# Performance work log

Measured on AMD Instinct MI355X. Metric: run time of the kernel, lower is better.

Reference implementation:

```python
import jax, jax.numpy as jnp
import numpy as np

EPS = 1e-5

def _rmsnorm(x, w):
    return x * jax.lax.rsqrt(jnp.mean(x * x, axis=-1, keepdims=True) + EPS) * w


def setup_inputs() -> dict:
    key = jax.random.key(0)
    ks = jax.random.split(key, 12)
    b, l, d = 2, 4096, 1024
    expand, d_state, d_conv, headdim = 2, 128, 4, 64
    d_inner = d * expand            # 2048
    nheads = d_inner // headdim     # 32
    conv_dim = d_inner + 2 * d_state            # 2304 (x, B, C; ngroups=1)
    d_in_proj = 2 * d_inner + 2 * d_state + nheads  # z, xBC, dt
    s = 0.02
    return {
        "x": jax.random.normal(ks[0], (b, l, d), jnp.float32),
        "norm_w": jnp.ones((d,), jnp.float32),
        "in_proj_W": jax.random.normal(ks[1], (d, d_in_proj), jnp.float32) * s,
        "conv_W": jax.random.normal(ks[2], (d_conv, conv_dim), jnp.float32) * s,
        "conv_b": jnp.zeros((conv_dim,), jnp.float32),
        "dt_bias": jax.random.normal(ks[3], (nheads,), jnp.float32) * 0.5,
        "A_log": jnp.log(jnp.arange(1, nheads + 1, dtype=jnp.float32)),
        "D": jnp.ones((nheads,), jnp.float32),
        "gnorm_w": jnp.ones((d_inner,), jnp.float32),
        "zero_W": jax.random.normal(ks[4], (d, d_inner), jnp.float32) * s,
        "one_W": jax.random.normal(ks[5], (d, d_inner), jnp.float32) * s,
        "fusion_W": jax.random.normal(ks[6], (3 * d_inner, d), jnp.float32) * s,
    }


def _mamba2(xn, in_proj_W, conv_W, conv_b, dt_bias, A_log, D, gnorm_w):
    b, l, _ = xn.shape
    nheads = dt_bias.shape[0]
    conv_dim = conv_W.shape[1]
    d_state = (conv_W.shape[1] - gnorm_w.shape[0]) // 2
    d_inner = gnorm_w.shape[0]
    headdim = d_inner // nheads

    zxbcdt = xn @ in_proj_W                         # (b,l, 2*d_inner+2*n+h)
    z = zxbcdt[..., :d_inner]
    xBC = zxbcdt[..., d_inner:d_inner + conv_dim]
    dt = zxbcdt[..., -nheads:]

    # causal depthwise conv over seq, kernel size d_conv
    d_conv = conv_W.shape[0]
    pad = jnp.pad(xBC, ((0, 0), (d_conv - 1, 0), (0, 0)))
    conv = conv_b
    for k in range(d_conv):
        conv = conv + pad[:, k:k + l, :] * conv_W[k]
    xBC = jax.nn.silu(conv)

    xs = xBC[..., :d_inner].reshape(b, l, nheads, headdim)   # (b,l,h,p)
    Bm = xBC[..., d_inner:d_inner + d_state]                 # (b,l,n)
    Cm = xBC[..., d_inner + d_state:]                        # (b,l,n)

    dt = jax.nn.softplus(dt + dt_bias)                       # (b,l,h)
    A = -jnp.exp(A_log)                                      # (h,)
    dA = jnp.exp(dt * A)                                     # (b,l,h)

    def step(state, inp):
        dA_t, dt_t, B_t, C_t, x_t = inp   # (b,h),(b,h),(b,n),(b,n),(b,h,p)
        state = state * dA_t[:, :, None, None] + \
            (dt_t[:, :, None] * x_t)[..., None] * B_t[:, None, None, :]
        y_t = jnp.einsum('bhpn,bn->bhp', state, C_t)
        return state, y_t

    state0 = jnp.zeros((b, nheads, headdim, d_state), xn.dtype)
    inps = (dA.transpose(1, 0, 2), dt.transpose(1, 0, 2),
            Bm.transpose(1, 0, 2), Cm.transpose(1, 0, 2),
            xs.transpose(1, 0, 2, 3))
    _, ys = jax.lax.scan(step, state0, inps)                 # (l,b,h,p)
    y = ys.transpose(1, 0, 2, 3) + D[None, None, :, None] * xs
    y = y.reshape(b, l, d_inner)
    return _rmsnorm(y * jax.nn.silu(z), gnorm_w)             # (b,l,d_inner)


def reference(x, norm_w, in_proj_W, conv_W, conv_b, dt_bias, A_log, D,
              gnorm_w, zero_W, one_W, fusion_W):
    residual = x
    xn = _rmsnorm(x, norm_w)
    mamba_out = _mamba2(xn, in_proj_W, conv_W, conv_b, dt_bias, A_log, D, gnorm_w)
    y_zero = xn @ zero_W
    y_one = jnp.cumsum(xn @ one_W, axis=1)
    fused = jnp.concatenate([mamba_out, y_zero, y_one], axis=-1)
    return residual + fused @ fusion_W
```

## Files before the change

### kernel.cpp

```cpp
#include <hip/hip_runtime.h>
#include <hip/hip_bf16.h>
#include <stdint.h>

#define BATCH   2
#define SEQL    4096
#define DMODEL  1024
#define DIN     2048
#define NH      32
#define HDIM    64
#define DSTATE  128
#define CONVD   2304
#define DPROJ   4384
#define NTOT    8192
#define NBIG    6528
#define NREAL   6432
#define CHT     128
#define NCH     32
#define SP      136

typedef __attribute__((ext_vector_type(8))) short short8;
typedef __attribute__((ext_vector_type(4))) float f32x4;

__device__ __forceinline__ unsigned short f2bf(float f) {
    unsigned int u = __builtin_bit_cast(unsigned int, f);
    return (unsigned short)((u + 0x7FFFu + ((u >> 16) & 1u)) >> 16);
}
__device__ __forceinline__ float bf2f(unsigned short u) {
    unsigned int v = ((unsigned int)u) << 16;
    return __builtin_bit_cast(float, v);
}

__device__ __forceinline__ void gload16(const void* g, void* l) {
    __builtin_amdgcn_global_load_lds(
        (const __attribute__((address_space(1))) unsigned int*)g,
        (__attribute__((address_space(3))) unsigned int*)l,
        16, 0, 0);
}

__global__ void transpose_cast_kernel(const float* __restrict__ in,
                                      unsigned short* __restrict__ out,
                                      int R, int C) {
    __shared__ float tile[32][33];
    int c0 = blockIdx.x * 32, r0 = blockIdx.y * 32;
    int tx = threadIdx.x, ty = threadIdx.y;
    #pragma unroll
    for (int i = ty; i < 32; i += 8)
        tile[i][tx] = in[(size_t)(r0 + i) * C + c0 + tx];
    __syncthreads();
    #pragma unroll
    for (int i = ty; i < 32; i += 8)
        out[(size_t)(c0 + i) * R + r0 + tx] = f2bf(tile[tx][i]);
}

__global__ void cast_bf16_kernel(const float* __restrict__ in,
                                 unsigned short* __restrict__ out, int n4) {
    int i = (blockIdx.x * 256 + threadIdx.x) * 4;
    if (i < n4) {
        float4 v = *(const float4*)(in + i);
        ushort4 o;
        o.x = f2bf(v.x); o.y = f2bf(v.y); o.z = f2bf(v.z); o.w = f2bf(v.w);
        *(ushort4*)(out + i) = o;
    }
}

__global__ void zero_pad_kernel(unsigned short* __restrict__ p, int n) {
    int i = blockIdx.x * 256 + threadIdx.x;
    if (i < n) p[i] = 0;
}

__global__ __launch_bounds__(256) void rmsnorm_cast_kernel(
    const float* __restrict__ x, const float* __restrict__ w,
    unsigned short* __restrict__ xn) {
    int tok = blockIdx.x, tid = threadIdx.x;
    float4 v = ((const float4*)(x + (size_t)tok * DMODEL))[tid];
    float ss = v.x*v.x + v.y*v.y + v.z*v.z + v.w*v.w;
    #pragma unroll
    for (int off = 32; off > 0; off >>= 1) ss += __shfl_xor(ss, off, 64);
    __shared__ float sred[4];
    if ((tid & 63) == 0) sred[tid >> 6] = ss;
    __syncthreads();
    float tot = sred[0] + sred[1] + sred[2] + sred[3];
    float r = rsqrtf(tot * (1.0f / DMODEL) + 1e-5f);
    float4 wv = ((const float4*)w)[tid];
    ushort4 o;
    o.x = f2bf(v.x * r * wv.x); o.y = f2bf(v.y * r * wv.y);
    o.z = f2bf(v.z * r * wv.z); o.w = f2bf(v.w * r * wv.w);
    ((ushort4*)(xn + (size_t)tok * DMODEL))[tid] = o;
}

template<int MODE>
__global__ __launch_bounds__(256) void gemm_bt_kernel(
    const unsigned short* __restrict__ A, int lda,
    const unsigned short* __restrict__ B, int ldb,
    void* __restrict__ Cout, int ldc, int K,
    const float* __restrict__ addX, const unsigned short* __restrict__ Zbuf) {
    __shared__ __align__(16) unsigned short sA[128 * 64];
    __shared__ __align__(16) unsigned short sB[128 * 64];
    int tid = threadIdx.x;
    int bid = blockIdx.y * gridDim.x + blockIdx.x;
    int W = gridDim.x * 8;
    int band = bid / W, rem = bid % W;
    int bn = rem >> 3, bm = band * 8 + (rem & 7);
    int wave = tid >> 6, lane = tid & 63;
    int wm = wave >> 1, wn = wave & 1;
    f32x4 acc[4][4] = {};
    const unsigned short* Ab = A + (size_t)(bm * 128) * lda;
    const unsigned short* Bb = B + (size_t)(bn * 128) * ldb;
    int sRow = tid >> 3;
    int srcoff = (((tid & 7) - (tid >> 3)) & 7) * 8;
    int quad = lane >> 4, l15 = lane & 15;
    for (int k0 = 0; k0 < K; k0 += 64) {
        __syncthreads();
        #pragma unroll
        for (int it = 0; it < 4; ++it) {
            int row = sRow + it * 32;
            gload16(&Ab[(size_t)row * lda + k0 + srcoff], &sA[it * 2048 + tid * 8]);
            gload16(&Bb[(size_t)row * ldb + k0 + srcoff], &sB[it * 2048 + tid * 8]);
        }
        __syncthreads();
        #pragma unroll
        for (int kk = 0; kk < 64; kk += 32) {
            short8 a[4], b[4];
            #pragma unroll
            for (int i = 0; i < 4; ++i) {
                int mr = wm * 64 + i * 16 + l15;
                a[i] = *(const short8*)&sA[mr * 64 + (((kk >> 3) + quad + mr) & 7) * 8];
                int nr = wn * 64 + i * 16 + l15;
                b[i] = *(const short8*)&sB[nr * 64 + (((kk >> 3) + quad + nr) & 7) * 8];
            }
            #pragma unroll
            for (int i = 0; i < 4; ++i)
                #pragma unroll
                for (int j = 0; j < 4; ++j)
                    acc[i][j] = __builtin_amdgcn_mfma_f32_16x16x32_bf16(
                        a[i], b[j], acc[i][j], 0, 0, 0);
        }
    }
    int rbase = bm * 128 + wm * 64 + quad * 4;
    int cbase = bn * 128 + wn * 64 + l15;
    #pragma unroll
    for (int i = 0; i < 4; ++i) {
        #pragma unroll
        for (int r = 0; r < 4; ++r) {
            int gr = rbase + i * 16 + r;
            if constexpr (MODE == 1) {
                unsigned short* crow = (unsigned short*)Cout + (size_t)gr * ldc + cbase;
                #pragma unroll
                for (int j = 0; j < 4; ++j) crow[j * 16] = f2bf(acc[i][j][r]);
            } else {
                float* crow = (float*)Cout + (size_t)gr * ldc + cbase;
                const float* xr = addX + (size_t)gr * DMODEL + cbase;
                const unsigned short* zrow = Zbuf + (size_t)gr * NBIG;
                const float* qrow = (const float*)zrow;
                #pragma unroll
                for (int j = 0; j < 4; ++j)
                    crow[j * 16] = acc[i][j][r] + xr[j * 16]
                                 + bf2f(zrow[4384 + cbase + j * 16])
                                 + qrow[cbase + j * 16];
            }
        }
    }
}

__global__ __launch_bounds__(256) void gemm64_kernel(
    const unsigned short* __restrict__ A, int lda,
    const unsigned short* __restrict__ B, int ldb,
    unsigned short* __restrict__ Cout, int ldc, int K) {
    __shared__ __align__(16) unsigned short sA[64 * 64];
    __shared__ __align__(16) unsigned short sB[64 * 64];
    int tid = threadIdx.x;
    int bn = blockIdx.x, bm = blockIdx.y;
    int wave = tid >> 6, lane = tid & 63;
    int wm = wave >> 1, wn = wave & 1;
    f32x4 acc[2][2] = {};
    const unsigned short* Ab = A + (size_t)(bm * 64) * lda;
    const unsigned short* Bb = B + (size_t)(bn * 64) * ldb;
    int sRow = tid >> 3;
    int srcoff = (((tid & 7) - (tid >> 3)) & 7) * 8;
    int quad = lane >> 4, l15 = lane & 15;
    for (int k0 = 0; k0 < K; k0 += 64) {
        __syncthreads();
        #pragma unroll
        for (int it = 0; it < 2; ++it) {
            int row = sRow + it * 32;
            gload16(&Ab[(size_t)row * lda + k0 + srcoff], &sA[it * 2048 + tid * 8]);
            gload16(&Bb[(size_t)row * ldb + k0 + srcoff], &sB[it * 2048 + tid * 8]);
        }
        __syncthreads();
        #pragma unroll
        for (int kk = 0; kk < 64; kk += 32) {
            short8 a[2], b[2];
            #pragma unroll
            for (int i = 0; i < 2; ++i) {
                int mr = wm * 32 + i * 16 + l15;
                a[i] = *(const short8*)&sA[mr * 64 + (((kk >> 3) + quad + mr) & 7) * 8];
                int nr = wn * 32 + i * 16 + l15;
                b[i] = *(const short8*)&sB[nr * 64 + (((kk >> 3) + quad + nr) & 7) * 8];
            }
            #pragma unroll
            for (int i = 0; i < 2; ++i)
                #pragma unroll
                for (int j = 0; j < 2; ++j)
                    acc[i][j] = __builtin_amdgcn_mfma_f32_16x16x32_bf16(
                        a[i], b[j], acc[i][j], 0, 0, 0);
        }
    }
    int rbase = bm * 64 + wm * 32 + quad * 4;
    int cbase = bn * 64 + wn * 32 + l15;
    #pragma unroll
    for (int i = 0; i < 2; ++i)
        #pragma unroll
        for (int r = 0; r < 4; ++r) {
            int gr = rbase + i * 16 + r;
            unsigned short* crow = Cout + (size_t)gr * ldc + cbase;
            #pragma unroll
            for (int j = 0; j < 2; ++j) crow[j * 16] = f2bf(acc[i][j][r]);
        }
}

__global__ __launch_bounds__(256) void conv_silu_kernel(
    const unsigned short* __restrict__ Z, const float* __restrict__ convW,
    const float* __restrict__ convB, unsigned short* __restrict__ xbc) {
    int tok = blockIdx.x;
    int bi = tok >> 12, t = tok & 4095;
    for (int c = threadIdx.x; c < CONVD; c += 256) {
        float acc = convB[c];
        #pragma unroll
        for (int k = 0; k < 4; ++k) {
            int tt = t - 3 + k;
            if (tt >= 0)
                acc += bf2f(Z[(size_t)(bi * SEQL + tt) * NBIG + 2048 + c]) * convW[k * CONVD + c];
        }
        xbc[(size_t)tok * CONVD + c] = f2bf(acc / (1.0f + expf(-acc)));
    }
}

__global__ __launch_bounds__(256, 2) void chunk_intra_kernel(
    const unsigned short* __restrict__ xbc, const unsigned short* __restrict__ Z,
    const float* __restrict__ dt_bias, const float* __restrict__ A_log,
    unsigned short* __restrict__ TS, float* __restrict__ abuf,
    unsigned short* __restrict__ ym) {
    __shared__ __align__(16) unsigned short Xt[64 * SP];
    __shared__ __align__(16) unsigned short Xw[64 * SP];
    __shared__ __align__(16) unsigned short BtM[128 * SP];
    __shared__ float dt_lds[128], dtA_lds[128], cum_lds[128], w_lds[128];
    int tid = threadIdx.x;
    int kch = blockIdx.x, bh = blockIdx.y;
    int h = bh & 31, bi = bh >> 5;
    int tok0 = bi * SEQL + kch * CHT;
    const unsigned short* xb = xbc + (size_t)tok0 * CONVD;
    if (tid < 128) {
        float v = bf2f(Z[(size_t)(tok0 + tid) * NBIG + 4352 + h]) + dt_bias[h];
        float sp = (v > 20.f) ? v : log1pf(expf(v));
        dt_lds[tid] = sp;
        dtA_lds[tid] = -sp * expf(A_log[h]);
    }
    for (int seg = tid; seg < 128 * 16; seg += 256) {
        int s = seg & 127, nb = seg >> 7;
        short8 v = *(const short8*)&xb[(size_t)s * CONVD + 2048 + nb * 8];
        #pragma unroll
        for (int j = 0; j < 8; ++j) BtM[(nb * 8 + j) * SP + s] = (unsigned short)v[j];
    }
    for (int seg = tid; seg < 128 * 8; seg += 256) {
        int s = seg & 127, pb = seg >> 7;
        short8 v = *(const short8*)&xb[(size_t)s * CONVD + h * 64 + pb * 8];
        #pragma unroll
        for (int j = 0; j < 8; ++j) Xt[(pb * 8 + j) * SP + s] = (unsigned short)v[j];
    }
    __syncthreads();
    if (tid < 128) {
        int lw = tid & 63;
        float v = dtA_lds[tid];
        #pragma unroll
        for (int off = 1; off < 64; off <<= 1) {
            float o = __shfl_up(v, off, 64);
            if (lw >= off) v += o;
        }
        cum_lds[tid] = v;
    }
    __syncthreads();
    if (tid >= 64 && tid < 128) cum_lds[tid] += cum_lds[63];
    __syncthreads();
    if (tid < 128) {
        float cT = cum_lds[127];
        w_lds[tid] = __expf(cT - cum_lds[tid]) * dt_lds[tid];
        abuf[(size_t)(bh * NCH + kch) * 128 + tid] = __expf(cum_lds[tid]);
    }
    __syncthreads();
    for (int seg = tid; seg < 64 * 16; seg += 256) {
        int pp = seg >> 4, sb = seg & 15;
        short8 v = *(const short8*)&Xt[pp * SP + sb * 8];
        short8 o;
        #pragma unroll
        for (int j = 0; j < 8; ++j)
            o[j] = (short)f2bf(bf2f((unsigned short)v[j]) * w_lds[sb * 8 + j]);
        *(short8*)&Xw[pp * SP + sb * 8] = o;
    }
    __syncthreads();
    int lane = tid & 63, wv = tid >> 6;
    int quad = lane >> 4, l15 = lane & 15;
    {
        f32x4 acc[8] = {};
        for (int kk = 0; kk < 128; kk += 32) {
            short8 a = *(const short8*)&Xw[(16 * wv + l15) * SP + kk + quad * 8];
            #pragma unroll
            for (int jn = 0; jn < 8; ++jn) {
                short8 b = *(const short8*)&BtM[(16 * jn + l15) * SP + kk + quad * 8];
                acc[jn] = __builtin_amdgcn_mfma_f32_16x16x32_bf16(a, b, acc[jn], 0, 0, 0);
            }
        }
        size_t tsbase = (size_t)(bh * NCH + kch) * 8192;
        #pragma unroll
        for (int jn = 0; jn < 8; ++jn)
            #pragma unroll
            for (int r = 0; r < 4; ++r) {
                int pp = 16 * wv + quad * 4 + r, n = 16 * jn + l15;
                TS[tsbase + pp * 128 + n] = f2bf(acc[jn][r]);
            }
    }
    __syncthreads();
    {
        f32x4 g[2][8] = {};
        for (int kk = 0; kk < 128; kk += 32) {
            int co = 2176 + kk + quad * 8;
            short8 a0 = *(const short8*)&xb[(size_t)(32 * wv + l15) * CONVD + co];
            short8 a1 = *(const short8*)&xb[(size_t)(32 * wv + 16 + l15) * CONVD + co];
            int bo = 2048 + kk + quad * 8;
            #pragma unroll
            for (int js = 0; js < 8; ++js) {
                short8 b = *(const short8*)&xb[(size_t)(16 * js + l15) * CONVD + bo];
                g[0][js] = __builtin_amdgcn_mfma_f32_16x16x32_bf16(a0, b, g[0][js], 0, 0, 0);
                g[1][js] = __builtin_amdgcn_mfma_f32_16x16x32_bf16(a1, b, g[1][js], 0, 0, 0);
            }
        }
        #pragma unroll
        for (int it = 0; it < 2; ++it)
            #pragma unroll
            for (int js = 0; js < 8; ++js) {
                int s = 16 * js + l15;
                float cs = cum_lds[s], ds = dt_lds[s];
                #pragma unroll
                for (int r = 0; r < 4; ++r) {
                    int t = 32 * wv + 16 * it + quad * 4 + r;
                    float f = (s <= t) ? __expf(cum_lds[t] - cs) * ds : 0.f;
                    BtM[t * SP + s] = f2bf(g[it][js][r] * f);
                }
            }
    }
    __syncthreads();
    {
        f32x4 y[2][4] = {};
        for (int kk = 0; kk < 128; kk += 32) {
            short8 a0 = *(const short8*)&BtM[(32 * wv + l15) * SP + kk + quad * 8];
            short8 a1 = *(const short8*)&BtM[(32 * wv + 16 + l15) * SP + kk + quad * 8];
            #pragma unroll
            for (int jp = 0; jp < 4; ++jp) {
                short8 b = *(const short8*)&Xt[(16 * jp + l15) * SP + kk + quad * 8];
                y[0][jp] = __builtin_amdgcn_mfma_f32_16x16x32_bf16(a0, b, y[0][jp], 0, 0, 0);
                y[1][jp] = __builtin_amdgcn_mfma_f32_16x16x32_bf16(a1, b, y[1][jp], 0, 0, 0);
            }
        }
        #pragma unroll
        for (int it = 0; it < 2; ++it)
            #pragma unroll
            for (int jp = 0; jp < 4; ++jp)
                #pragma unroll
                for (int r = 0; r < 4; ++r) {
                    int t = 32 * wv + 16 * it + quad * 4 + r;
                    int pp = 16 * jp + l15;
                    ym[(size_t)(tok0 + t) * DIN + h * 64 + pp] = f2bf(y[it][jp][r]);
                }
    }
}

__global__ __launch_bounds__(128) void state_recur_kernel(
    unsigned short* __restrict__ TS, const float* __restrict__ abuf) {
    int bh = blockIdx.x >> 6, p = blockIdx.x & 63, n = threadIdx.x;
    float s = 0.f;
    for (int k = 0; k < NCH; ++k) {
        size_t base = ((size_t)(bh * NCH + k) * 64 + p) * 128 + n;
        float aT = abuf[(size_t)(bh * NCH + k) * 128 + 127];
        float tv = bf2f(TS[base]);
        TS[base] = f2bf(s);
        s = fmaf(aT, s, tv);
    }
}

__global__ __launch_bounds__(256) void chunk_inter_kernel(
    const unsigned short* __restrict__ xbc, const unsigned short* __restrict__ TS,
    const float* __restrict__ abuf, const float* __restrict__ Dp,
    unsigned short* ym) {
    __shared__ float a_ld[128];
    int tid = threadIdx.x;
    int kch = blockIdx.x, bh = blockIdx.y;
    int h = bh & 31, bi = bh >> 5;
    int tok0 = bi * SEQL + kch * CHT;
    if (tid < 128) a_ld[tid] = abuf[(size_t)(bh * NCH + kch) * 128 + tid];
    __syncthreads();
    int lane = tid & 63, wv = tid >> 6;
    int quad = lane >> 4, l15 = lane & 15;
    const unsigned short* xb = xbc + (size_t)tok0 * CONVD;
    size_t tsbase = (size_t)(bh * NCH + kch) * 8192;
    int t0 = 32 * wv + l15, t1 = t0 + 16;
    float at0 = a_ld[t0], at1 = a_ld[t1];
    f32x4 y[2][4] = {};
    for (int kk = 0; kk < 128; kk += 32) {
        int co = 2176 + kk + quad * 8;
        short8 c0 = *(const short8*)&xb[(size_t)t0 * CONVD + co];
        short8 c1 = *(const short8*)&xb[(size_t)t1 * CONVD + co];
        short8 a0, a1;
        #pragma unroll
        for (int j = 0; j < 8; ++j) {
            a0[j] = (short)f2bf(bf2f((unsigned short)c0[j]) * at0);
            a1[j] = (short)f2bf(bf2f((unsigned short)c1[j]) * at1);
        }
        #pragma unroll
        for (int jp = 0; jp < 4; ++jp) {
            short8 b = *(const short8*)&TS[tsbase + (size_t)(16 * jp + l15) * 128 + kk + quad * 8];
            y[0][jp] = __builtin_amdgcn_mfma_f32_16x16x32_bf16(a0, b, y[0][jp], 0, 0, 0);
            y[1][jp] = __builtin_amdgcn_mfma_f32_16x16x32_bf16(a1, b, y[1][jp], 0, 0, 0);
        }
    }
    float Dh = Dp[h];
    #pragma unroll
    for (int it = 0; it < 2; ++it)
        #pragma unroll
        for (int jp = 0; jp < 4; ++jp)
            #pragma unroll
            for (int r = 0; r < 4; ++r) {
                int t = 32 * wv + 16 * it + quad * 4 + r;
                int pp = 16 * jp + l15;
                size_t yi = (size_t)(tok0 + t) * DIN + h * 64 + pp;
                float xv = bf2f(xb[(size_t)t * CONVD + h * 64 + pp]);
                float yv = y[it][jp][r] + bf2f(ym[yi]) + Dh * xv;
                ym[yi] = f2bf(yv);
            }
}

__global__ __launch_bounds__(256) void gated_norm_kernel(
    const unsigned short* __restrict__ y,
    const unsigned short* __restrict__ Z,
    const float* __restrict__ gw, unsigned short* mamba) {
    int tok = blockIdx.x, tid = threadIdx.x;
    float vals[8];
    float ss = 0;
    #pragma unroll
    for (int i = 0; i < 8; ++i) {
        int c = tid + i * 256;
        float yv = bf2f(y[(size_t)tok * DIN + c]);
        float zv = bf2f(Z[(size_t)tok * NBIG + c]);
        float g = yv * (zv / (1.0f + expf(-zv)));
        vals[i] = g;
        ss += g * g;
    }
    #pragma unroll
    for (int off = 32; off > 0; off >>= 1) ss += __shfl_xor(ss, off, 64);
    __shared__ float sred[4];
    if ((tid & 63) == 0) sred[tid >> 6] = ss;
    __syncthreads();
    float tot = sred[0] + sred[1] + sred[2] + sred[3];
    float r = rsqrtf(tot * (1.0f / DIN) + 1e-5f);
    #pragma unroll
    for (int i = 0; i < 8; ++i) {
        int c = tid + i * 256;
        mamba[(size_t)tok * DIN + c] = f2bf(vals[i] * r * gw[c]);
    }
}

__global__ void cumsum_pass1_kernel(const unsigned short* __restrict__ Z,
                                    float* __restrict__ S) {
    int cg = blockIdx.x & 3, ch = (blockIdx.x >> 2) & 31, bi = blockIdx.x >> 7;
    int c = cg * 256 + threadIdx.x;
    size_t base = (size_t)(bi * SEQL + ch * 128) * NBIG;
    float s = 0;
    for (int t = 0; t < 128; ++t)
        s += bf2f(Z[base + (size_t)t * NBIG + 5408 + c]);
    S[(bi * 32 + ch) * 1024 + c] = s;
}

__global__ void cumsum_pass2_kernel(unsigned short* __restrict__ Z,
                                    const float* __restrict__ S) {
    int cg = blockIdx.x & 3, ch = (blockIdx.x >> 2) & 31, bi = blockIdx.x >> 7;
    int c = cg * 256 + threadIdx.x;
    float run = 0;
    for (int k = 0; k < ch; ++k) run += S[(bi * 32 + k) * 1024 + c];
    size_t base = (size_t)(bi * SEQL + ch * 128) * NBIG;
    for (int t = 0; t < 128; ++t) {
        size_t row = base + (size_t)t * NBIG;
        run += bf2f(Z[row + 5408 + c]);
        ((float*)(Z + row))[c] = run;
    }
}

extern "C" void kernel_launch(void* const* d_in, const int* in_sizes, int n_in,
                              void* d_out, int out_size, void* d_ws, size_t ws_size,
                              hipStream_t stream) {
    (void)in_sizes; (void)n_in; (void)out_size; (void)ws_size;
    const float* x        = (const float*)d_in[0];
    const float* norm_w   = (const float*)d_in[1];
    const float* in_projW = (const float*)d_in[2];
    const float* conv_W   = (const float*)d_in[3];
    const float* conv_b   = (const float*)d_in[4];
    const float* dt_bias  = (const float*)d_in[5];
    const float* A_log    = (const float*)d_in[6];
    const float* Dp       = (const float*)d_in[7];
    const float* gnorm_w  = (const float*)d_in[8];
    const float* zero_W   = (const float*)d_in[9];
    const float* one_W    = (const float*)d_in[10];
    const float* fusion_W = (const float*)d_in[11];
    float* out = (float*)d_out;

    char* p = (char*)d_ws;
    auto alloc = [&](size_t bytes) { char* r = p; p += (bytes + 255) & ~(size_t)255; return r; };
    unsigned short* Wf_t  = (unsigned short*)alloc((size_t)DMODEL * 6144 * 2);
    char* pool0 = p;
    unsigned short* xn_bf = (unsigned short*)alloc((size_t)NTOT * DMODEL * 2);
    unsigned short* zWb   = (unsigned short*)alloc((size_t)DMODEL * DIN * 2);
    unsigned short* oWb   = (unsigned short*)alloc((size_t)DMODEL * DIN * 2);
    unsigned short* Bt    = (unsigned short*)alloc((size_t)NBIG * DMODEL * 2);
    unsigned short* xbc   = (unsigned short*)pool0;
    float* abuf = (float*)alloc((size_t)64 * NCH * 128 * 4);
    float* Sb   = (float*)alloc((size_t)2 * 32 * 1024 * 4);
    unsigned short* ym  = (unsigned short*)alloc((size_t)NTOT * DIN * 2);
    unsigned short* Zbf = (unsigned short*)alloc((size_t)NTOT * NBIG * 2);
    unsigned short* TS = (unsigned short*)d_out;

    transpose_cast_kernel<<<dim3(DPROJ / 32, DMODEL / 32), dim3(32, 8), 0, stream>>>(
        in_projW, Bt, DMODEL, DPROJ);
    transpose_cast_kernel<<<dim3(DMODEL / 32, 6144 / 32), dim3(32, 8), 0, stream>>>(
        fusion_W, Wf_t, 6144, DMODEL);
    cast_bf16_kernel<<<2048, 256, 0, stream>>>(zero_W, zWb, DMODEL * DIN);
    cast_bf16_kernel<<<2048, 256, 0, stream>>>(one_W, oWb, DMODEL * DIN);
    zero_pad_kernel<<<384, 256, 0, stream>>>(
        Bt + (size_t)NREAL * DMODEL, (NBIG - NREAL) * DMODEL);

    rmsnorm_cast_kernel<<<NTOT, 256, 0, stream>>>(x, norm_w, xn_bf);

    gemm64_kernel<<<dim3(16, 16), 256, 0, stream>>>(
        Wf_t + 2048, 6144, zWb, DIN, Bt + (size_t)4384 * DMODEL, DMODEL, DIN);
    gemm64_kernel<<<dim3(16, 16), 256, 0, stream>>>(
        Wf_t + 4096, 6144, oWb, DIN, Bt + (size_t)5408 * DMODEL, DMODEL, DIN);

    gemm_bt_kernel<1><<<dim3(NBIG / 128, NTOT / 128), 256, 0, stream>>>(
        xn_bf, DMODEL, Bt, DMODEL, Zbf, NBIG, DMODEL, nullptr, nullptr);

    conv_silu_kernel<<<NTOT, 256, 0, stream>>>(Zbf, conv_W, conv_b, xbc);

    chunk_intra_kernel<<<dim3(NCH, 64), 256, 0, stream>>>(
        xbc, Zbf, dt_bias, A_log, TS, abuf, ym);
    state_recur_kernel<<<64 * 64, 128, 0, stream>>>(TS, abuf);
    chunk_inter_kernel<<<dim3(NCH, 64), 256, 0, stream>>>(
        xbc, TS, abuf, Dp, ym);

    gated_norm_kernel<<<NTOT, 256, 0, stream>>>(ym, Zbf, gnorm_w, ym);

    cumsum_pass1_kernel<<<256, 256, 0, stream>>>(Zbf, Sb);
    cumsum_pass2_kernel<<<256, 256, 0, stream>>>(Zbf, Sb);

    gemm_bt_kernel<2><<<dim3(DMODEL / 128, NTOT / 128), 256, 0, stream>>>(
        ym, DIN, Wf_t, 6144, out, DMODEL, DIN, x, Zbf);
}
```

Measured before the change: 664.3 us.

## Replace big input projection GEMM with 256x256-tile, 512-thread pipelined MFMA kernel

Replaces the 128x128-tile gemm_bt_kernel for the large xn @ [in_proj | fused weights] GEMM with a new 256x256-tile kernel using 8 waves, an 8-slot LDS ring fed by global_load_lds, swizzled LDS layout, XCD-aware block remapping, and s_setprio around MFMA bursts. The weight buffer is padded to 6656 columns so the N dimension divides by 256, and stores are masked past the real column count. The goal is higher arithmetic intensity and better overlap of loads and MFMA. The cost is higher register and LDS pressure (128KB LDS per block), and some wasted compute on padded columns.

Result: faster. 642.0 us (-3.3%).

```diff
diff --git a/kernel.cpp b/kernel.cpp
--- a/kernel.cpp
+++ b/kernel.cpp
@@ -14,6 +14,7 @@
 #define NTOT    8192
 #define NBIG    6528
 #define NREAL   6432
+#define NPAD    6656
 #define CHT     128
 #define NCH     32
 #define SP      136
@@ -86,6 +87,107 @@
     o.x = f2bf(v.x * r * wv.x); o.y = f2bf(v.y * r * wv.y);
     o.z = f2bf(v.z * r * wv.z); o.w = f2bf(v.w * r * wv.w);
     ((ushort4*)(xn + (size_t)tok * DMODEL))[tid] = o;
+}
+
+__global__ __launch_bounds__(512, 2) void gemm256_kernel(
+    const unsigned short* __restrict__ A, int lda,
+    const unsigned short* __restrict__ B, int ldb,
+    unsigned short* __restrict__ Cout, int ldc, int K, int Nreal) {
+    __shared__ __align__(16) unsigned short lds[8][8192];
+    const int tid = threadIdx.x;
+    const int nkt = K >> 6;
+    const int ghalves = nkt << 2;
+
+    int nwg = gridDim.x * gridDim.y;
+    int orig = blockIdx.y * gridDim.x + blockIdx.x;
+    int q8 = nwg >> 3;
+    int wgid = (orig & 7) * q8 + (orig >> 3);
+    int W = gridDim.x * 4;
+    int band = wgid / W, rem = wgid % W;
+    int bm = band * 4 + (rem & 3), bn = rem >> 2;
+
+    const int wave = tid >> 6, lane = tid & 63;
+    const int wm = wave >> 2, wn = wave & 3;
+    const int quad = lane >> 4, l15 = lane & 15;
+    const int cpos = (((l15 & 1) << 2) + quad + (l15 >> 1)) & 7;
+    const int aoff = wm * 4096 + (l15 >> 1) * 64 + cpos * 8;
+    const int boff = wn * 2048 + (l15 >> 1) * 64 + cpos * 8;
+
+    const int srow = tid >> 3;
+    const int dch  = tid & 7;
+    const int ech  = (dch - srow) & 7;
+    const int g_r0 = 2 * srow + (ech >> 2);
+    const int g_c0 = (ech & 3) * 8;
+    const unsigned short* A0 = A + (size_t)(bm * 256 + g_r0) * lda + g_c0;
+    const unsigned short* A1 = A0 + (size_t)128 * lda;
+    const unsigned short* B0 = B + (size_t)(bn * 256 + g_r0) * ldb + g_c0;
+    const unsigned short* B1 = B0 + (size_t)128 * ldb;
+
+    auto stage = [&](int g) {
+        int tg = g >> 2, idx = g & 3;
+        int k0 = tg * 64 + ((idx >> 1) << 5);
+        unsigned short* d = &lds[g & 7][tid * 8];
+        if (idx & 1) { gload16(B0 + k0, d); gload16(B1 + k0, d + 4096); }
+        else         { gload16(A0 + k0, d); gload16(A1 + k0, d + 4096); }
+    };
+
+    f32x4 acc[8][4] = {};
+    stage(0); stage(1); stage(2); stage(3);
+    asm volatile("s_waitcnt vmcnt(4)");
+    stage(4); stage(5); stage(6);
+    asm volatile("s_waitcnt vmcnt(6)");
+    __builtin_amdgcn_s_barrier();
+
+    short8 a[8], b[2];
+    for (int t = 0; t < nkt; ++t) {
+        #pragma unroll
+        for (int ph = 0; ph < 4; ++ph) {
+            const int kk = ph >> 1, nq = ph & 1;
+            const unsigned short* As = lds[(4 * t + 2 * kk) & 7];
+            const unsigned short* Bs = lds[(4 * t + 2 * kk + 1) & 7];
+            if (nq == 0) {
+                #pragma unroll
+                for (int m = 0; m < 8; ++m)
+                    a[m] = *(const short8*)&As[aoff + m * 512];
+            }
+            b[0] = *(const short8*)&Bs[boff + (nq * 2) * 512];
+            b[1] = *(const short8*)&Bs[boff + (nq * 2 + 1) * 512];
+            int g = 4 * t + 7 + ph;
+            if (g < ghalves) stage(g);
+            __builtin_amdgcn_s_barrier();
+            asm volatile("s_waitcnt lgkmcnt(0)");
+            __builtin_amdgcn_s_setprio(1);
+            #pragma unroll
+            for (int m = 0; m < 8; ++m) {
+                acc[m][nq * 2]     = __builtin_amdgcn_mfma_f32_16x16x32_bf16(
+                    a[m], b[0], acc[m][nq * 2], 0, 0, 0);
+                acc[m][nq * 2 + 1] = __builtin_amdgcn_mfma_f32_16x16x32_bf16(
+                    a[m], b[1], acc[m][nq * 2 + 1], 0, 0, 0);
+            }
+            __builtin_amdgcn_s_setprio(0);
+            if (ph == 3) {
+                if (t == nkt - 2) asm volatile("s_waitcnt vmcnt(0)");
+                else              asm volatile("s_waitcnt vmcnt(6)");
+            }
+            __builtin_amdgcn_s_barrier();
+        }
+    }
+
+    const int rbase = bm * 256 + wm * 128 + quad * 4;
+    const int cb0 = bn * 256 + wn * 64 + l15;
+    #pragma unroll
+    for (int m = 0; m < 8; ++m) {
+        #pragma unroll
+        for (int n = 0; n < 4; ++n) {
+            int cb = cb0 + n * 16;
+            if (cb < Nreal) {
+                unsigned short* cp = Cout + (size_t)(rbase + m * 16) * ldc + cb;
+                #pragma unroll
+                for (int r = 0; r < 4; ++r)
+                    cp[(size_t)r * ldc] = f2bf(acc[m][n][r]);
+            }
+        }
+    }
 }
 
 template<int MODE>
@@ -517,7 +619,7 @@
     unsigned short* xn_bf = (unsigned short*)alloc((size_t)NTOT * DMODEL * 2);
     unsigned short* zWb   = (unsigned short*)alloc((size_t)DMODEL * DIN * 2);
     unsigned short* oWb   = (unsigned short*)alloc((size_t)DMODEL * DIN * 2);
-    unsigned short* Bt    = (unsigned short*)alloc((size_t)NBIG * DMODEL * 2);
+    unsigned short* Bt    = (unsigned short*)alloc((size_t)NPAD * DMODEL * 2);
     unsigned short* xbc   = (unsigned short*)pool0;
     float* abuf = (float*)alloc((size_t)64 * NCH * 128 * 4);
     float* Sb   = (float*)alloc((size_t)2 * 32 * 1024 * 4);
@@ -531,8 +633,8 @@
         fusion_W, Wf_t, 6144, DMODEL);
     cast_bf16_kernel<<<2048, 256, 0, stream>>>(zero_W, zWb, DMODEL * DIN);
     cast_bf16_kernel<<<2048, 256, 0, stream>>>(one_W, oWb, DMODEL * DIN);
-    zero_pad_kernel<<<384, 256, 0, stream>>>(
-        Bt + (size_t)NREAL * DMODEL, (NBIG - NREAL) * DMODEL);
+    zero_pad_kernel<<<(NPAD - NREAL) * DMODEL / 256, 256, 0, stream>>>(
+        Bt + (size_t)NREAL * DMODEL, (NPAD - NREAL) * DMODEL);
 
     rmsnorm_cast_kernel<<<NTOT, 256, 0, stream>>>(x, norm_w, xn_bf);
 
@@ -541,8 +643,8 @@
     gemm64_kernel<<<dim3(16, 16), 256, 0, stream>>>(
         Wf_t + 4096, 6144, oWb, DIN, Bt + (size_t)5408 * DMODEL, DMODEL, DIN);
 
-    gemm_bt_kernel<1><<<dim3(NBIG / 128, NTOT / 128), 256, 0, stream>>>(
-        xn_bf, DMODEL, Bt, DMODEL, Zbf, NBIG, DMODEL, nullptr, nullptr);
+    gemm256_kernel<<<dim3(NPAD / 256, NTOT / 256), 512, 0, stream>>>(
+        xn_bf, DMODEL, Bt, DMODEL, Zbf, NBIG, DMODEL, NBIG);
 
     conv_silu_kernel<<<NTOT, 256, 0, stream>>>(Zbf, conv_W, conv_b, xbc);
 
```
